# Kernel tuning notes

Hardware: AMD Instinct MI355X
Metric: run time of the kernel (lower is better)

Reference implementation:

```python
import jax, jax.numpy as jnp
import numpy as np

GEN_POLY = ("1011011", "1111001")  # constraint_length 7, rate 1/2
LARGE = 1e9  # metric for infeasible start states


def _build_trellis(gen_poly):
    """Static trellis tables (numpy, built at trace time).

    State = last mu input bits (most recent bit is MSB), matching the
    shift-register convention: next_state = [u, s_bits[:-1]].
    """
    conv_n = len(gen_poly)
    K = len(gen_poly[0])
    mu = K - 1
    ns, ni, no = 2 ** mu, 2, 2 ** conv_n
    g = np.array([[int(c) for c in p] for p in gen_poly])  # (conv_n, K)
    to_nodes = np.zeros((ns, ni), np.int32)
    op = np.zeros((ns, ni), np.int32)
    for s in range(ns):
        s_bits = [(s >> (mu - 1 - i)) & 1 for i in range(mu)]
        for u in range(ni):
            reg = np.array([u] + s_bits)          # [u_t, u_{t-1}, ..., u_{t-mu}]
            outs = (g @ reg) % 2                  # conv_n output bits
            op[s, u] = int("".join(map(str, outs)), 2)
            to_nodes[s, u] = int("".join(map(str, [u] + s_bits[:-1])), 2)
    from_nodes = np.zeros((ns, ni), np.int32)
    op_by_tonode = np.zeros((ns, ni), np.int32)
    cnt = np.zeros(ns, np.int32)
    for s in range(ns):
        for u in range(ni):
            t = to_nodes[s, u]
            from_nodes[t, cnt[t]] = s
            op_by_tonode[t, cnt[t]] = op[s, u]
            cnt[t] += 1
    op_bits = np.array([[(o >> (conv_n - 1 - j)) & 1 for j in range(conv_n)]
                        for o in range(no)], np.float32)  # (no, conv_n)
    return conv_n, ns, ni, to_nodes, from_nodes, op_by_tonode, op_bits


def setup_inputs() -> dict:
    key = jax.random.key(0)
    # noisy channel LLRs for B=512 codewords of length n=4096
    inputs = jax.random.normal(key, (512, 4096), dtype=jnp.float32) * 2.0
    return {"inputs": inputs}


def reference(inputs):
    conv_n, ns, ni, to_nodes_np, from_nodes_np, op_by_tonode_np, op_bits = \
        _build_trellis(GEN_POLY)
    tn = jnp.asarray(to_nodes_np)       # (ns, ni) next state
    fn = jnp.asarray(from_nodes_np)     # (ns, ni) predecessor states
    opt = jnp.asarray(op_by_tonode_np)  # (ns, ni) output symbol on that branch

    B, n = inputs.shape
    T = n // conv_n                     # number of trellis steps / info bits
    y = inputs.reshape(B, T, conv_n)

    # soft_llr branch metrics: bm[t,b,o] = sum_c y[b,t,c] * (1 - 2*op_bit[o,c])
    sign = jnp.asarray(1.0 - 2.0 * op_bits)          # (no, conv_n)
    bm = jnp.einsum('btc,oc->tbo', y, sign)          # (T, B, no)

    cum0 = jnp.full((B, ns), LARGE, jnp.float32).at[:, 0].set(0.0)
    st_rng = jnp.arange(ns)

    def acs(cum, bm_t):
        # add: metric of (prev_state i, output symbol j)
        sm = bm_t[:, None, :] + cum[:, :, None]      # (B, ns, no)
        # gather by to-node: candidates for each next state
        cand = sm[:, fn, opt]                        # (B, ns, ni)
        j = jnp.argmin(cand, axis=2)                 # compare-select
        tb = fn[st_rng[None, :], j]                  # traceback predecessor (B, ns)
        cum_t = jnp.min(cand, axis=2)
        return cum_t, (cum_t, tb)

    cum_T, (cms, tbs) = jax.lax.scan(acs, cum0, bm)  # tbs: (T, B, ns)

    # traceback from optimal terminal state
    term = jnp.argmin(cum_T, axis=1).astype(jnp.int32)

    def tb_step(st, tb_t):
        prev = jnp.take_along_axis(tb_t, st[:, None], axis=1)[:, 0]
        return prev, st

    p0, ys = jax.lax.scan(tb_step, term, tbs[1:], reverse=True)
    # path states at times 0..T (initial state is 0)
    paths = jnp.concatenate(
        [jnp.zeros((B, 1), jnp.int32), p0[:, None], jnp.swapaxes(ys, 0, 1)],
        axis=1)                                       # (B, T+1)

    # recover input bit per transition: bit u s.t. to_nodes[prev, u] == next
    match = tn[paths[:, :-1]] == paths[:, 1:][:, :, None]  # (B, T, ni)
    bits = jnp.sum(jnp.where(match, jnp.arange(ni, dtype=jnp.int32), 0), axis=-1)
    return bits.astype(jnp.float32)                   # (B, T) hard bit estimates
```

## Files before the change

### kernel.cpp

```cpp
#include <hip/hip_runtime.h>
#include <stdint.h>

#define T_STEPS 2048
#define NCHUNK  86
#define LARGEF  1.0e9f
#define NB      512
typedef unsigned long long u64;
typedef unsigned uint2v __attribute__((ext_vector_type(2)));

__device__ __forceinline__ int par6(int x) { return __builtin_popcount((unsigned)x) & 1; }

constexpr int CARR[6] = {5, 6, 12, 8, 16, 32};

template<int CTRL>
__device__ __forceinline__ float xdpp(float x) {
  return __int_as_float(__builtin_amdgcn_update_dpp(0, __float_as_int(x), CTRL, 0xF, 0xF, true));
}
template<int CTRL>
__device__ __forceinline__ unsigned xdpp_u(unsigned x) {
  return (unsigned)__builtin_amdgcn_update_dpp(0, (int)x, CTRL, 0xF, 0xF, true);
}
__device__ __forceinline__ unsigned selmask_u(unsigned a_false, unsigned b_true, u64 m) {
  unsigned out;
  asm("v_cndmask_b32 %0, %1, %2, %3" : "=v"(out) : "v"(a_false), "v"(b_true), "s"(m));
  return out;
}
__device__ __forceinline__ unsigned exch16_u(unsigned x, u64 mrx) {
#if __has_builtin(__builtin_amdgcn_permlane16_swap)
  uint2v r = __builtin_amdgcn_permlane16_swap(x, x, false, false);
  return selmask_u(r.y, r.x, mrx);
#else
  (void)mrx;
  return (unsigned)__builtin_amdgcn_ds_swizzle((int)x, 0x401F);
#endif
}
__device__ __forceinline__ unsigned exch32_u(unsigned x, u64 mrx) {
#if __has_builtin(__builtin_amdgcn_permlane32_swap)
  uint2v r = __builtin_amdgcn_permlane32_swap(x, x, false, false);
  return selmask_u(r.y, r.x, mrx);
#else
  (void)mrx;
  return (unsigned)__shfl_xor((int)x, 32, 64);
#endif
}
template<int PH>
__device__ __forceinline__ float exchf(float x, const u64 (&mrx)[2]) {
  if constexpr (PH == 0) return xdpp<0xB1>(x);
  else if constexpr (PH == 1) return xdpp<0x4E>(x);
  else if constexpr (PH == 2) return xdpp<0x141>(x);
  else if constexpr (PH == 3) return xdpp<0x140>(x);
  else if constexpr (PH == 4) return __uint_as_float(exch16_u(__float_as_uint(x), mrx[0]));
  else return __uint_as_float(exch32_u(__float_as_uint(x), mrx[1]));
}
template<int PH>
__device__ __forceinline__ unsigned exchu(unsigned x, const u64 (&mrx)[2]) {
  if constexpr (PH == 0) return xdpp_u<0xB1>(x);
  else if constexpr (PH == 1) return xdpp_u<0x4E>(x);
  else if constexpr (PH == 2) return xdpp_u<0x141>(x);
  else if constexpr (PH == 3) return xdpp_u<0x140>(x);
  else if constexpr (PH == 4) return exch16_u(x, mrx[0]);
  else return exch32_u(x, mrx[1]);
}

struct Phc {
  float sae[6], sbe[6];
  unsigned sgn[6];
  unsigned pdu[6];
  u64 pdm[6];
  u64 mrx[2];
};

__device__ __forceinline__ void mk_sasb(int lane, int ph, float& sae, float& sbe, int& pdv) {
  pdv = par6(lane & CARR[ph]);
  int t = 0;
#pragma unroll
  for (int j = 0; j < 5; ++j) t |= par6(lane & CARR[(ph + 1 + j) % 6]) << j;
  t |= pdv << 5;
  const float sa = 1.0f - 2.0f * (float)par6(t & 45);
  const float sb = 1.0f - 2.0f * (float)par6(t & 60);
  sae = pdv ? -sa : sa;
  sbe = pdv ? -sb : sb;
}

__device__ __forceinline__ void mk_mrx(int lane, u64 (&mrx)[2]) {
  const u64 ODD16 = 0xFFFF0000FFFF0000ull, HI32 = 0xFFFFFFFF00000000ull;
#if __has_builtin(__builtin_amdgcn_permlane16_swap)
  {
    uint2v r = __builtin_amdgcn_permlane16_swap((unsigned)lane, (unsigned)lane, false, false);
    mrx[0] = (((unsigned)__builtin_amdgcn_readlane((int)r.x, 0) == 16u)) ? ~ODD16 : ODD16;
  }
#else
  mrx[0] = 0;
#endif
#if __has_builtin(__builtin_amdgcn_permlane32_swap)
  {
    uint2v r = __builtin_amdgcn_permlane32_swap((unsigned)lane, (unsigned)lane, false, false);
    mrx[1] = (((unsigned)__builtin_amdgcn_readlane((int)r.x, 0) == 32u)) ? ~HI32 : HI32;
  }
#else
  mrx[1] = 0;
#endif
}

__device__ __forceinline__ void mkconsts(int lane, Phc& p) {
#pragma unroll
  for (int ph = 0; ph < 6; ++ph) {
    int pdv;
    mk_sasb(lane, ph, p.sae[ph], p.sbe[ph], pdv);
    p.sgn[ph] = pdv ? 0u : 0x80000000u;
    p.pdu[ph] = (unsigned)pdv;
    p.pdm[ph] = __ballot(pdv != 0);
  }
  mk_mrx(lane, p.mrx);
}

template<int N>
__device__ __forceinline__ void bmcalc(const float4 (&fy)[12], float (&bm)[24],
                                       const float (&sae)[6], const float (&sbe)[6]) {
#pragma unroll
  for (int k = 0; k < N; ++k) {
    const int ph = k % 6;
    const float y0 = (k & 1) ? fy[k >> 1].z : fy[k >> 1].x;
    const float y1 = (k & 1) ? fy[k >> 1].w : fy[k >> 1].y;
    bm[k] = fmaf(sae[ph], y0, sbe[ph] * y1);
  }
}

template<int N, int K>
__device__ __forceinline__ void acs(float& cum, unsigned& dw, const float (&bm)[24],
                                    const unsigned (&sgn)[6], const u64 (&mrx)[2]) {
  if constexpr (K < N) {
    constexpr int ph = K % 6;
    const float ex = exchf<ph>(cum, mrx);
    const float cA = cum + bm[K];
    const float cB = ex - bm[K];
    const float D = cA - cB;
    cum = fminf(cA, cB);
    unsigned tmp;
    asm("v_xor_b32 %0, %2, %3\n\t"
        "v_cmp_gt_f32 vcc, 0, %0\n\t"
        "v_addc_co_u32 %1, vcc, %1, %1, vcc"
        : "=&v"(tmp), "+v"(dw)
        : "v"(D), "v"(sgn[ph]) : "vcc");
    acs<N, K + 1>(cum, dw, bm, sgn, mrx);
  }
}

template<int N, int K>
__device__ __forceinline__ void wrec(unsigned& word, unsigned& dws, const unsigned (&pdu)[6],
                                     const u64 (&pdm)[6], const u64 (&mrx)[2]) {
  if constexpr (K < N) {
    constexpr int ph = K % 6;
    const unsigned exw = exchu<ph>(word, mrx);
    asm("v_cmp_gt_i32 vcc, 0, %1\n\t"
        "v_add_u32 %1, %1, %1\n\t"
        "s_xor_b64 vcc, vcc, %3\n\t"
        "v_cndmask_b32 %0, %0, %2, vcc"
        : "+v"(word), "+v"(dws)
        : "v"(exw), "s"(pdm[ph]) : "vcc");
    word |= pdu[ph] << (6 + K);
    wrec<N, K + 1>(word, dws, pdu, pdm, mrx);
  }
}

__device__ __forceinline__ int term_argmin(float cum, int lane) {
  const int stf = par6(lane & 12) | (par6(lane & 8) << 1) | (par6(lane & 16) << 2) |
                  (par6(lane & 32) << 3) | (par6(lane & 5) << 4) | (par6(lane & 6) << 5);
  float v = cum; int bs = stf; int bl = lane;
#pragma unroll
  for (int off = 32; off >= 1; off >>= 1) {
    const float ov = __shfl_xor(v, off, 64);
    const int os = __shfl_xor(bs, off, 64);
    const int ol = __shfl_xor(bl, off, 64);
    if (ov < v || (ov == v && os < bs)) { v = ov; bs = os; bl = ol; }
  }
  return bl;
}

__global__ __launch_bounds__(64, 1) void vit_fwd(const float* __restrict__ in,
                                                 unsigned* __restrict__ dwg,
                                                 int* __restrict__ term) {
  __shared__ float y_lds[2 * T_STEPS];
  const int b = blockIdx.x;
  const int lane = threadIdx.x;
  {
    const float4* g = (const float4*)(in + (size_t)b * (2 * T_STEPS));
    float4* l = (float4*)y_lds;
#pragma unroll
    for (int i = 0; i < 16; ++i) l[i * 64 + lane] = g[i * 64 + lane];
  }
  __syncthreads();

  Phc p;
  mkconsts(lane, p);

  float cum = (lane == 0) ? 0.0f : LARGEF;
  float bm[24];
  float4 cur[12], nxt[12];
  const float4* y4 = (const float4*)y_lds;
  unsigned* dwp = dwg + (size_t)b * (NCHUNK * 64) + lane;
  unsigned dw;
#pragma unroll
  for (int j = 0; j < 12; ++j) cur[j] = y4[j];
  for (int cc = 0; cc < 42; ++cc) {
    const int c0 = 2 * cc;
    bmcalc<24>(cur, bm, p.sae, p.sbe);
#pragma unroll
    for (int j = 0; j < 12; ++j) nxt[j] = y4[12 * (c0 + 1) + j];
    dw = 0; acs<24, 0>(cum, dw, bm, p.sgn, p.mrx);
    *dwp = dw; dwp += 64;
    bmcalc<24>(nxt, bm, p.sae, p.sbe);
#pragma unroll
    for (int j = 0; j < 12; ++j) cur[j] = y4[12 * (c0 + 2) + j];
    dw = 0; acs<24, 0>(cum, dw, bm, p.sgn, p.mrx);
    *dwp = dw; dwp += 64;
  }
  bmcalc<24>(cur, bm, p.sae, p.sbe);
#pragma unroll
  for (int j = 0; j < 4; ++j) nxt[j] = y4[1020 + j];
  dw = 0; acs<24, 0>(cum, dw, bm, p.sgn, p.mrx);
  *dwp = dw; dwp += 64;
  bmcalc<8>(nxt, bm, p.sae, p.sbe);
  dw = 0; acs<8, 0>(cum, dw, bm, p.sgn, p.mrx);
  *dwp = dw;

  const int bl = term_argmin(cum, lane);
  if (lane == 0) term[b] = bl;
}

__global__ __launch_bounds__(512, 1) void vit_rc(const unsigned* __restrict__ dwg,
                                                 const int* __restrict__ term,
                                                 float* __restrict__ out) {
  __shared__ unsigned tbf[NCHUNK][64];
  const int tid = threadIdx.x;
  const int lane = tid & 63;
  const int wv = tid >> 6;
  const int b = blockIdx.x;

  unsigned pdu[6];
  u64 pdm[6], mrx[2];
#pragma unroll
  for (int ph = 0; ph < 6; ++ph) {
    const int pdv = par6(lane & CARR[ph]);
    pdu[ph] = (unsigned)pdv;
    pdm[ph] = __ballot(pdv != 0);
  }
  mk_mrx(lane, mrx);

  const int cbeg = wv * 11;
  const int cend = (cbeg + 11 < NCHUNK) ? cbeg + 11 : NCHUNK;
  for (int c = cbeg; c < cend; ++c) {
    const unsigned dw = dwg[((size_t)b * NCHUNK + c) * 64 + lane];
    unsigned word = (unsigned)lane;
    if (c == NCHUNK - 1) {
      unsigned dws = dw << 24;
      wrec<8, 0>(word, dws, pdu, pdm, mrx);
    } else {
      unsigned dws = dw << 8;
      wrec<24, 0>(word, dws, pdu, pdm, mrx);
    }
    tbf[c][lane] = word;
  }
  __syncthreads();

  if (wv == 0) {
    int lam = __builtin_amdgcn_readfirstlane(term[b]);
    const size_t ob = (size_t)b * T_STEPS;
    unsigned row = tbf[NCHUNK - 1][lane];
    for (int c = NCHUNK - 1; c >= 0; --c) {
      unsigned nrow = 0;
      if (c > 0) nrow = tbf[c - 1][lane];
      const unsigned w = (unsigned)__builtin_amdgcn_readlane((int)row, lam);
      const int nb = (c == NCHUNK - 1) ? 8 : 24;
      if (lane < nb) out[ob + c * 24 + lane] = (float)((w >> (6 + lane)) & 1u);
      lam = (int)(w & 63u);
      row = nrow;
    }
  }
}

template<int N, int K>
__device__ __forceinline__ void fb_step(float& cum, unsigned& word, const float (&bm)[24],
                                        const Phc& p) {
  if constexpr (K < N) {
    constexpr int ph = K % 6;
    const float ex = exchf<ph>(cum, p.mrx);
    const unsigned exw = exchu<ph>(word, p.mrx);
    const float cA = cum + bm[K];
    const float cB = ex - bm[K];
    const float D = cA - cB;
    cum = fminf(cA, cB);
    const unsigned w0 = selmask_u(word, exw, p.pdm[ph]);
    const unsigned w1 = selmask_u(exw, word, p.pdm[ph]);
    const bool d = __uint_as_float(__float_as_uint(D) ^ p.sgn[ph]) < 0.0f;
    word = (d ? w1 : w0) | (p.pdu[ph] << (6 + K));
    fb_step<N, K + 1>(cum, word, bm, p);
  }
}
__global__ __launch_bounds__(64, 1) void vit_fb(const float* __restrict__ in,
                                                float* __restrict__ out) {
  __shared__ float y_lds[2 * T_STEPS];
  __shared__ unsigned tbf[NCHUNK][64];
  const int b = blockIdx.x;
  const int lane = threadIdx.x;
  {
    const float4* g = (const float4*)(in + (size_t)b * (2 * T_STEPS));
    float4* l = (float4*)y_lds;
#pragma unroll
    for (int i = 0; i < 16; ++i) l[i * 64 + lane] = g[i * 64 + lane];
  }
  __syncthreads();
  Phc p;
  mkconsts(lane, p);
  float cum = (lane == 0) ? 0.0f : LARGEF;
  unsigned word = (unsigned)lane;
  float bm[24];
  float4 cur[12], nxt[12];
  const float4* y4 = (const float4*)y_lds;
#pragma unroll
  for (int j = 0; j < 12; ++j) cur[j] = y4[j];
  for (int cc = 0; cc < 42; ++cc) {
    const int c0 = 2 * cc;
    bmcalc<24>(cur, bm, p.sae, p.sbe);
#pragma unroll
    for (int j = 0; j < 12; ++j) nxt[j] = y4[12 * (c0 + 1) + j];
    fb_step<24, 0>(cum, word, bm, p);
    tbf[c0][lane] = word; word = (unsigned)lane;
    bmcalc<24>(nxt, bm, p.sae, p.sbe);
#pragma unroll
    for (int j = 0; j < 12; ++j) cur[j] = y4[12 * (c0 + 2) + j];
    fb_step<24, 0>(cum, word, bm, p);
    tbf[c0 + 1][lane] = word; word = (unsigned)lane;
  }
  bmcalc<24>(cur, bm, p.sae, p.sbe);
#pragma unroll
  for (int j = 0; j < 4; ++j) nxt[j] = y4[1020 + j];
  fb_step<24, 0>(cum, word, bm, p);
  tbf[84][lane] = word; word = (unsigned)lane;
  bmcalc<8>(nxt, bm, p.sae, p.sbe);
  fb_step<8, 0>(cum, word, bm, p);
  tbf[85][lane] = word;

  int lam = __builtin_amdgcn_readfirstlane(term_argmin(cum, lane));
  const size_t ob = (size_t)b * T_STEPS;
  unsigned row = tbf[85][lane];
  for (int c = 85; c >= 0; --c) {
    unsigned nrow = 0;
    if (c > 0) nrow = tbf[c - 1][lane];
    const unsigned w = (unsigned)__builtin_amdgcn_readlane((int)row, lam);
    const int nb = (c == 85) ? 8 : 24;
    if (lane < nb) out[ob + c * 24 + lane] = (float)((w >> (6 + lane)) & 1u);
    lam = (int)(w & 63u);
    row = nrow;
  }
}

extern "C" void kernel_launch(void* const* d_in, const int* in_sizes, int n_in,
                              void* d_out, int out_size, void* d_ws, size_t ws_size,
                              hipStream_t stream) {
  const float* in = (const float*)d_in[0];
  float* out = (float*)d_out;
  (void)in_sizes; (void)n_in; (void)out_size;
  const size_t nwords = (size_t)NB * NCHUNK * 64;
  const size_t need = nwords * 4 + NB * 4;
  if (ws_size >= need) {
    unsigned* dwg = (unsigned*)d_ws;
    int* term = (int*)(dwg + nwords);
    vit_fwd<<<dim3(NB), dim3(64), 0, stream>>>(in, dwg, term);
    vit_rc<<<dim3(NB), dim3(512), 0, stream>>>(dwg, term, out);
  } else {
    vit_fb<<<dim3(NB), dim3(64), 0, stream>>>(in, out);
  }
}
```

Before: 70.20 us.

## Fuse forward ACS and traceback into one 512-thread kernel; use v_cmp_class for decisions

Result: faster. 66.36 us (-5.5%).

```diff
diff --git a/kernel.cpp b/kernel.cpp
--- a/kernel.cpp
+++ b/kernel.cpp
@@ -64,7 +64,7 @@
 
 struct Phc {
   float sae[6], sbe[6];
-  unsigned sgn[6];
+  unsigned clsm[6];
   unsigned pdu[6];
   u64 pdm[6];
   u64 mrx[2];
@@ -107,7 +107,7 @@
   for (int ph = 0; ph < 6; ++ph) {
     int pdv;
     mk_sasb(lane, ph, p.sae[ph], p.sbe[ph], pdv);
-    p.sgn[ph] = pdv ? 0u : 0x80000000u;
+    p.clsm[ph] = pdv ? 0x01Cu : 0x380u;
     p.pdu[ph] = (unsigned)pdv;
     p.pdm[ph] = __ballot(pdv != 0);
   }
@@ -128,7 +128,7 @@
 
 template<int N, int K>
 __device__ __forceinline__ void acs(float& cum, unsigned& dw, const float (&bm)[24],
-                                    const unsigned (&sgn)[6], const u64 (&mrx)[2]) {
+                                    const unsigned (&clsm)[6], const u64 (&mrx)[2]) {
   if constexpr (K < N) {
     constexpr int ph = K % 6;
     const float ex = exchf<ph>(cum, mrx);
@@ -136,13 +136,10 @@
     const float cB = ex - bm[K];
     const float D = cA - cB;
     cum = fminf(cA, cB);
-    unsigned tmp;
-    asm("v_xor_b32 %0, %2, %3\n\t"
-        "v_cmp_gt_f32 vcc, 0, %0\n\t"
-        "v_addc_co_u32 %1, vcc, %1, %1, vcc"
-        : "=&v"(tmp), "+v"(dw)
-        : "v"(D), "v"(sgn[ph]) : "vcc");
-    acs<N, K + 1>(cum, dw, bm, sgn, mrx);
+    asm("v_cmp_class_f32 vcc, %1, %2\n\t"
+        "v_addc_co_u32 %0, vcc, %0, %0, vcc"
+        : "+v"(dw) : "v"(D), "v"(clsm[ph]) : "vcc");
+    acs<N, K + 1>(cum, dw, bm, clsm, mrx);
   }
 }
 
@@ -177,99 +174,87 @@
   return bl;
 }
 
-__global__ __launch_bounds__(64, 1) void vit_fwd(const float* __restrict__ in,
-                                                 unsigned* __restrict__ dwg,
-                                                 int* __restrict__ term) {
+__global__ __launch_bounds__(512, 1) void vit_all(const float* __restrict__ in,
+                                                  float* __restrict__ out) {
   __shared__ float y_lds[2 * T_STEPS];
-  const int b = blockIdx.x;
-  const int lane = threadIdx.x;
-  {
-    const float4* g = (const float4*)(in + (size_t)b * (2 * T_STEPS));
-    float4* l = (float4*)y_lds;
-#pragma unroll
-    for (int i = 0; i < 16; ++i) l[i * 64 + lane] = g[i * 64 + lane];
-  }
-  __syncthreads();
-
-  Phc p;
-  mkconsts(lane, p);
-
-  float cum = (lane == 0) ? 0.0f : LARGEF;
-  float bm[24];
-  float4 cur[12], nxt[12];
-  const float4* y4 = (const float4*)y_lds;
-  unsigned* dwp = dwg + (size_t)b * (NCHUNK * 64) + lane;
-  unsigned dw;
-#pragma unroll
-  for (int j = 0; j < 12; ++j) cur[j] = y4[j];
-  for (int cc = 0; cc < 42; ++cc) {
-    const int c0 = 2 * cc;
-    bmcalc<24>(cur, bm, p.sae, p.sbe);
-#pragma unroll
-    for (int j = 0; j < 12; ++j) nxt[j] = y4[12 * (c0 + 1) + j];
-    dw = 0; acs<24, 0>(cum, dw, bm, p.sgn, p.mrx);
-    *dwp = dw; dwp += 64;
-    bmcalc<24>(nxt, bm, p.sae, p.sbe);
-#pragma unroll
-    for (int j = 0; j < 12; ++j) cur[j] = y4[12 * (c0 + 2) + j];
-    dw = 0; acs<24, 0>(cum, dw, bm, p.sgn, p.mrx);
-    *dwp = dw; dwp += 64;
-  }
-  bmcalc<24>(cur, bm, p.sae, p.sbe);
-#pragma unroll
-  for (int j = 0; j < 4; ++j) nxt[j] = y4[1020 + j];
-  dw = 0; acs<24, 0>(cum, dw, bm, p.sgn, p.mrx);
-  *dwp = dw; dwp += 64;
-  bmcalc<8>(nxt, bm, p.sae, p.sbe);
-  dw = 0; acs<8, 0>(cum, dw, bm, p.sgn, p.mrx);
-  *dwp = dw;
-
-  const int bl = term_argmin(cum, lane);
-  if (lane == 0) term[b] = bl;
-}
-
-__global__ __launch_bounds__(512, 1) void vit_rc(const unsigned* __restrict__ dwg,
-                                                 const int* __restrict__ term,
-                                                 float* __restrict__ out) {
-  __shared__ unsigned tbf[NCHUNK][64];
+  __shared__ unsigned buf[NCHUNK][64];
+  __shared__ int lam_sh;
+
   const int tid = threadIdx.x;
   const int lane = tid & 63;
   const int wv = tid >> 6;
   const int b = blockIdx.x;
 
-  unsigned pdu[6];
-  u64 pdm[6], mrx[2];
-#pragma unroll
-  for (int ph = 0; ph < 6; ++ph) {
-    const int pdv = par6(lane & CARR[ph]);
-    pdu[ph] = (unsigned)pdv;
-    pdm[ph] = __ballot(pdv != 0);
-  }
-  mk_mrx(lane, mrx);
-
-  const int cbeg = wv * 11;
-  const int cend = (cbeg + 11 < NCHUNK) ? cbeg + 11 : NCHUNK;
-  for (int c = cbeg; c < cend; ++c) {
-    const unsigned dw = dwg[((size_t)b * NCHUNK + c) * 64 + lane];
-    unsigned word = (unsigned)lane;
-    if (c == NCHUNK - 1) {
-      unsigned dws = dw << 24;
-      wrec<8, 0>(word, dws, pdu, pdm, mrx);
-    } else {
-      unsigned dws = dw << 8;
-      wrec<24, 0>(word, dws, pdu, pdm, mrx);
+  {
+    const float4* g = (const float4*)(in + (size_t)b * (2 * T_STEPS));
+    float4* l = (float4*)y_lds;
+    l[tid] = g[tid];
+    l[tid + 512] = g[tid + 512];
+  }
+  Phc p;
+  mkconsts(lane, p);
+  __syncthreads();
+
+  if (wv == 0) {
+    float cum = (lane == 0) ? 0.0f : LARGEF;
+    float bm[24];
+    float4 cur[12], nxt[12];
+    const float4* y4 = (const float4*)y_lds;
+    unsigned dw;
+#pragma unroll
+    for (int j = 0; j < 12; ++j) cur[j] = y4[j];
+    for (int cc = 0; cc < 42; ++cc) {
+      const int c0 = 2 * cc;
+      bmcalc<24>(cur, bm, p.sae, p.sbe);
+#pragma unroll
+      for (int j = 0; j < 12; ++j) nxt[j] = y4[12 * (c0 + 1) + j];
+      dw = 0; acs<24, 0>(cum, dw, bm, p.clsm, p.mrx);
+      buf[c0][lane] = dw;
+      bmcalc<24>(nxt, bm, p.sae, p.sbe);
+#pragma unroll
+      for (int j = 0; j < 12; ++j) cur[j] = y4[12 * (c0 + 2) + j];
+      dw = 0; acs<24, 0>(cum, dw, bm, p.clsm, p.mrx);
+      buf[c0 + 1][lane] = dw;
     }
-    tbf[c][lane] = word;
+    bmcalc<24>(cur, bm, p.sae, p.sbe);
+#pragma unroll
+    for (int j = 0; j < 4; ++j) nxt[j] = y4[1020 + j];
+    dw = 0; acs<24, 0>(cum, dw, bm, p.clsm, p.mrx);
+    buf[84][lane] = dw;
+    bmcalc<8>(nxt, bm, p.sae, p.sbe);
+    dw = 0; acs<8, 0>(cum, dw, bm, p.clsm, p.mrx);
+    buf[85][lane] = dw;
+
+    const int bl = term_argmin(cum, lane);
+    if (lane == 0) lam_sh = bl;
   }
   __syncthreads();
 
+  {
+    const int cbeg = wv * 11;
+    const int cend = (cbeg + 11 < NCHUNK) ? cbeg + 11 : NCHUNK;
+    for (int c = cbeg; c < cend; ++c) {
+      const unsigned dw = buf[c][lane];
+      unsigned word = (unsigned)lane;
+      if (c == NCHUNK - 1) {
+        unsigned dws = dw << 24;
+        wrec<8, 0>(word, dws, p.pdu, p.pdm, p.mrx);
+      } else {
+        unsigned dws = dw << 8;
+        wrec<24, 0>(word, dws, p.pdu, p.pdm, p.mrx);
+      }
+      buf[c][lane] = word;
+    }
+  }
+  __syncthreads();
+
   if (wv == 0) {
-    int lam = __builtin_amdgcn_readfirstlane(term[b]);
+    int lam = __builtin_amdgcn_readfirstlane(lam_sh);
     const size_t ob = (size_t)b * T_STEPS;
-    unsigned row = tbf[NCHUNK - 1][lane];
+    unsigned row = buf[NCHUNK - 1][lane];
     for (int c = NCHUNK - 1; c >= 0; --c) {
       unsigned nrow = 0;
-      if (c > 0) nrow = tbf[c - 1][lane];
+      if (c > 0) nrow = buf[c - 1][lane];
       const unsigned w = (unsigned)__builtin_amdgcn_readlane((int)row, lam);
       const int nb = (c == NCHUNK - 1) ? 8 : 24;
       if (lane < nb) out[ob + c * 24 + lane] = (float)((w >> (6 + lane)) & 1u);
@@ -279,96 +264,11 @@
   }
 }
 
-template<int N, int K>
-__device__ __forceinline__ void fb_step(float& cum, unsigned& word, const float (&bm)[24],
-                                        const Phc& p) {
-  if constexpr (K < N) {
-    constexpr int ph = K % 6;
-    const float ex = exchf<ph>(cum, p.mrx);
-    const unsigned exw = exchu<ph>(word, p.mrx);
-    const float cA = cum + bm[K];
-    const float cB = ex - bm[K];
-    const float D = cA - cB;
-    cum = fminf(cA, cB);
-    const unsigned w0 = selmask_u(word, exw, p.pdm[ph]);
-    const unsigned w1 = selmask_u(exw, word, p.pdm[ph]);
-    const bool d = __uint_as_float(__float_as_uint(D) ^ p.sgn[ph]) < 0.0f;
-    word = (d ? w1 : w0) | (p.pdu[ph] << (6 + K));
-    fb_step<N, K + 1>(cum, word, bm, p);
-  }
-}
-__global__ __launch_bounds__(64, 1) void vit_fb(const float* __restrict__ in,
-                                                float* __restrict__ out) {
-  __shared__ float y_lds[2 * T_STEPS];
-  __shared__ unsigned tbf[NCHUNK][64];
-  const int b = blockIdx.x;
-  const int lane = threadIdx.x;
-  {
-    const float4* g = (const float4*)(in + (size_t)b * (2 * T_STEPS));
-    float4* l = (float4*)y_lds;
-#pragma unroll
-    for (int i = 0; i < 16; ++i) l[i * 64 + lane] = g[i * 64 + lane];
-  }
-  __syncthreads();
-  Phc p;
-  mkconsts(lane, p);
-  float cum = (lane == 0) ? 0.0f : LARGEF;
-  unsigned word = (unsigned)lane;
-  float bm[24];
-  float4 cur[12], nxt[12];
-  const float4* y4 = (const float4*)y_lds;
-#pragma unroll
-  for (int j = 0; j < 12; ++j) cur[j] = y4[j];
-  for (int cc = 0; cc < 42; ++cc) {
-    const int c0 = 2 * cc;
-    bmcalc<24>(cur, bm, p.sae, p.sbe);
-#pragma unroll
-    for (int j = 0; j < 12; ++j) nxt[j] = y4[12 * (c0 + 1) + j];
-    fb_step<24, 0>(cum, word, bm, p);
-    tbf[c0][lane] = word; word = (unsigned)lane;
-    bmcalc<24>(nxt, bm, p.sae, p.sbe);
-#pragma unroll
-    for (int j = 0; j < 12; ++j) cur[j] = y4[12 * (c0 + 2) + j];
-    fb_step<24, 0>(cum, word, bm, p);
-    tbf[c0 + 1][lane] = word; word = (unsigned)lane;
-  }
-  bmcalc<24>(cur, bm, p.sae, p.sbe);
-#pragma unroll
-  for (int j = 0; j < 4; ++j) nxt[j] = y4[1020 + j];
-  fb_step<24, 0>(cum, word, bm, p);
-  tbf[84][lane] = word; word = (unsigned)lane;
-  bmcalc<8>(nxt, bm, p.sae, p.sbe);
-  fb_step<8, 0>(cum, word, bm, p);
-  tbf[85][lane] = word;
-
-  int lam = __builtin_amdgcn_readfirstlane(term_argmin(cum, lane));
-  const size_t ob = (size_t)b * T_STEPS;
-  unsigned row = tbf[85][lane];
-  for (int c = 85; c >= 0; --c) {
-    unsigned nrow = 0;
-    if (c > 0) nrow = tbf[c - 1][lane];
-    const unsigned w = (unsigned)__builtin_amdgcn_readlane((int)row, lam);
-    const int nb = (c == 85) ? 8 : 24;
-    if (lane < nb) out[ob + c * 24 + lane] = (float)((w >> (6 + lane)) & 1u);
-    lam = (int)(w & 63u);
-    row = nrow;
-  }
-}
-
 extern "C" void kernel_launch(void* const* d_in, const int* in_sizes, int n_in,
                               void* d_out, int out_size, void* d_ws, size_t ws_size,
                               hipStream_t stream) {
   const float* in = (const float*)d_in[0];
   float* out = (float*)d_out;
-  (void)in_sizes; (void)n_in; (void)out_size;
-  const size_t nwords = (size_t)NB * NCHUNK * 64;
-  const size_t need = nwords * 4 + NB * 4;
-  if (ws_size >= need) {
-    unsigned* dwg = (unsigned*)d_ws;
-    int* term = (int*)(dwg + nwords);
-    vit_fwd<<<dim3(NB), dim3(64), 0, stream>>>(in, dwg, term);
-    vit_rc<<<dim3(NB), dim3(512), 0, stream>>>(dwg, term, out);
-  } else {
-    vit_fb<<<dim3(NB), dim3(64), 0, stream>>>(in, out);
-  }
-}
+  (void)in_sizes; (void)n_in; (void)out_size; (void)d_ws; (void)ws_size;
+  vit_all<<<dim3(NB), dim3(512), 0, stream>>>(in, out);
+}
```
